# Kernel optimization log

Hardware: AMD Instinct MI355X
Metric: run time of the kernel (lower is better)

## Reference

```python
import jax, jax.numpy as jnp
import numpy as np

NUM_HEADS = 4
NUM_GROUPS = 8
EPS = 1e-5


def group_norm(x, gamma, beta):
    B, C, H, W = x.shape
    xg = x.reshape(B, NUM_GROUPS, C // NUM_GROUPS, H, W)
    mean = xg.mean(axis=(2, 3, 4), keepdims=True)
    var = xg.var(axis=(2, 3, 4), keepdims=True)
    xn = ((xg - mean) * jax.lax.rsqrt(var + EPS)).reshape(B, C, H, W)
    return xn * gamma[None, :, None, None] + beta[None, :, None, None]


def setup_inputs() -> dict:
    key = jax.random.key(0)
    k1, k2, k3 = jax.random.split(key, 3)
    B, C, H, W = 16, 512, 32, 32
    x = jax.random.normal(k1, (B, C, H, W), dtype=jnp.float32)
    gn_gamma = jnp.ones((C,), dtype=jnp.float32)
    gn_beta = jnp.zeros((C,), dtype=jnp.float32)
    w_qkv = jax.random.normal(k2, (3 * C, C), dtype=jnp.float32) * 0.02
    w_proj = jax.random.normal(k3, (C, C), dtype=jnp.float32) * 0.02
    b_proj = jnp.zeros((C,), dtype=jnp.float32)
    return {"x": x, "gn_gamma": gn_gamma, "gn_beta": gn_beta,
            "w_qkv": w_qkv, "w_proj": w_proj, "b_proj": b_proj}


def reference(x, gn_gamma, gn_beta, w_qkv, w_proj, b_proj):
    B, C, H, W = x.shape
    nh = NUM_HEADS
    hd = C // nh
    N = H * W

    x_norm = group_norm(x, gn_gamma, gn_beta)
    # 1x1 conv == channel matmul: (B,C,H,W) x (3C,C) -> (B,3C,H,W)
    qkv = jnp.einsum('bchw,dc->bdhw', x_norm, w_qkv)
    qkv = qkv.reshape(B, 3, nh, hd, N)
    q, k, v = qkv[:, 0], qkv[:, 1], qkv[:, 2]  # each (B, nh, hd, N)

    scale = hd ** (-0.5)
    attn = jnp.einsum('bhci,bhcj->bhij', q, k) * scale  # (B, nh, N, N)
    attn = jax.nn.softmax(attn, axis=-1)
    out = jnp.einsum('bhij,bhcj->bhci', attn, v)  # (B, nh, hd, N)
    out = out.reshape(B, C, H, W)

    proj = jnp.einsum('bchw,dc->bdhw', out, w_proj) + b_proj[None, :, None, None]
    return x + proj
```

## Files before the change

kernel.cpp:

```cpp
#include <hip/hip_runtime.h>
#include <stdint.h>

typedef unsigned short u16;
typedef unsigned int u32;
typedef __attribute__((ext_vector_type(8))) short short8;
typedef __attribute__((ext_vector_type(4))) float f32x4;
typedef __attribute__((ext_vector_type(16))) float f32x16;
typedef __attribute__((ext_vector_type(4))) u32 u32x4;

#define BATCH 16
#define CCH   512
#define NPIX  1024
#define NGRP  8
#define CPG   64
#define NHEAD 4
#define HDIM  128
#define KVBLK 64

__device__ __forceinline__ u16 f2bf(float f) {
  union { float f; u32 u; } v; v.f = f;
  u32 u = v.u;
  u32 r = (u + 0x7FFFu + ((u >> 16) & 1u)) >> 16;
  return (u16)r;
}

__device__ __forceinline__ void gload16(const void* g, void* l) {
  typedef __attribute__((address_space(3))) u32 L;
  typedef __attribute__((address_space(1))) const u32 G;
  __builtin_amdgcn_global_load_lds((G*)(uintptr_t)g, (L*)(u32)(uintptr_t)l, 16, 0, 0);
}

#define CVTPK(dst, a, b) asm("v_cvt_pk_bf16_f32 %0, %1, %2" : "=v"(dst) : "v"(a), "v"(b))
#define PLSWAP(a, b) asm("v_permlane32_swap_b32 %0, %1" : "+v"(a), "+v"(b))

__device__ __forceinline__ short8 rd512(const char* base, int r, int ck, int hi) {
  int byte = ((r >> 2) * 512) +
             ((((r & 3) * 128) + ck * 32 + hi * 16) ^ (((r >> 2) & 15) << 4));
  return *reinterpret_cast<const short8*>(base + byte);
}

__device__ __forceinline__ float softmax_pack(const f32x16& s0, const f32x16& s1, short8* pf) {
  float ps[4] = {0.f, 0.f, 0.f, 0.f};
  u32 pw[16];
  #pragma unroll
  for (int u = 0; u < 8; ++u) {
    float pa = exp2f(s0[2*u]);  float pb = exp2f(s0[2*u+1]);
    float pc = exp2f(s1[2*u]);  float pd = exp2f(s1[2*u+1]);
    ps[u & 3] += (pa + pb) + (pc + pd);
    CVTPK(pw[u],     pa, pb);
    CVTPK(pw[8 + u], pc, pd);
  }
  PLSWAP(pw[0], pw[2]);  PLSWAP(pw[1], pw[3]);
  PLSWAP(pw[4], pw[6]);  PLSWAP(pw[5], pw[7]);
  PLSWAP(pw[8], pw[10]); PLSWAP(pw[9], pw[11]);
  PLSWAP(pw[12], pw[14]); PLSWAP(pw[13], pw[15]);
  #pragma unroll
  for (int f = 0; f < 4; ++f) {
    u32x4 t = {pw[f*4], pw[f*4+1], pw[f*4+2], pw[f*4+3]};
    pf[f] = __builtin_bit_cast(short8, t);
  }
  float psum = (ps[0] + ps[1]) + (ps[2] + ps[3]);
  psum += __shfl_xor(psum, 32);
  return psum;
}

__global__ void gn_stats_k(const float* __restrict__ x, float* __restrict__ part) {
  int bg = blockIdx.x >> 3, sl = blockIdx.x & 7;
  const float* p = x + (size_t)bg * (CPG * NPIX) + sl * 8192;
  float s = 0.f, ss = 0.f;
  for (int i = threadIdx.x; i < 2048; i += 256) {
    float4 v = reinterpret_cast<const float4*>(p)[i];
    s  += v.x + v.y + v.z + v.w;
    ss += v.x*v.x + v.y*v.y + v.z*v.z + v.w*v.w;
  }
  for (int o = 32; o > 0; o >>= 1) { s += __shfl_down(s, o); ss += __shfl_down(ss, o); }
  __shared__ float sh[8];
  int wid = threadIdx.x >> 6;
  if ((threadIdx.x & 63) == 0) { sh[wid*2] = s; sh[wid*2+1] = ss; }
  __syncthreads();
  if (threadIdx.x == 0) {
    part[blockIdx.x*2]   = sh[0]+sh[2]+sh[4]+sh[6];
    part[blockIdx.x*2+1] = sh[1]+sh[3]+sh[5]+sh[7];
  }
}

__global__ __launch_bounds__(256) void gn_apply_t(const float* __restrict__ x,
                                                  const float* __restrict__ gamma,
                                                  const float* __restrict__ beta,
                                                  const float* __restrict__ part,
                                                  u16* __restrict__ xnT) {
  const int p0 = blockIdx.x * 64;
  const int c0 = blockIdx.y * 64;
  const int b  = blockIdx.z;
  __shared__ float lt[64][66];

  const int bg = b * NGRP + (c0 >> 6);
  float s = 0.f, ss = 0.f;
  #pragma unroll
  for (int k2 = 0; k2 < 8; ++k2) { s += part[(bg*8 + k2)*2]; ss += part[(bg*8 + k2)*2 + 1]; }
  const float invn = 1.f / (float)(CPG * NPIX);
  const float mean = s * invn;
  const float rstd = rsqrtf(ss * invn - mean * mean + 1e-5f);

  const int t = threadIdx.x;
  #pragma unroll
  for (int pass = 0; pass < 4; ++pass) {
    int c   = c0 + (t >> 4) + pass * 16;
    int pix = p0 + (t & 15) * 4;
    float ga = gamma[c] * rstd;
    float be = beta[c] - mean * ga;
    float4 v = *reinterpret_cast<const float4*>(&x[((size_t)(b*CCH + c)) * NPIX + pix]);
    int pl = (t & 15) * 4, cl = (t >> 4) + pass * 16;
    lt[pl+0][cl] = v.x*ga + be;
    lt[pl+1][cl] = v.y*ga + be;
    lt[pl+2][cl] = v.z*ga + be;
    lt[pl+3][cl] = v.w*ga + be;
  }
  __syncthreads();
  const int pl = t >> 2, cq = (t & 3) * 16;
  u32 wbuf[8];
  #pragma unroll
  for (int e = 0; e < 8; ++e) {
    u16 lo = f2bf(lt[pl][cq + e*2]);
    u16 hi = f2bf(lt[pl][cq + e*2 + 1]);
    wbuf[e] = (u32)lo | ((u32)hi << 16);
  }
  u32* dst = (u32*)&xnT[((size_t)(b*NPIX + p0 + pl)) * CCH + c0 + cq];
  #pragma unroll
  for (int e = 0; e < 8; ++e) dst[e] = wbuf[e];
}

__global__ void f2bf_all(const float* __restrict__ wqkv, const float* __restrict__ wproj,
                         u16* __restrict__ wq, u16* __restrict__ wp, float qs) {
  int i = blockIdx.x * 256 + threadIdx.x;
  float4 v; u16* dst; float sc = 1.f;
  if (i < 196608) {
    v = reinterpret_cast<const float4*>(wqkv)[i];
    if (i < 65536) sc = qs;
    dst = wq + (size_t)i * 4;
  } else {
    v = reinterpret_cast<const float4*>(wproj)[i - 196608];
    dst = wp + (size_t)(i - 196608) * 4;
  }
  u32 lo = (u32)f2bf(v.x*sc) | ((u32)f2bf(v.y*sc) << 16);
  u32 hi = (u32)f2bf(v.z*sc) | ((u32)f2bf(v.w*sc) << 16);
  *reinterpret_cast<uint2*>(dst) = make_uint2(lo, hi);
}

__global__ __launch_bounds__(256, 2) void gemm_qkv(const u16* __restrict__ xnT,
                                                   const u16* __restrict__ wq_bf,
                                                   u16* __restrict__ outQ,
                                                   u16* __restrict__ outK,
                                                   u16* __restrict__ outV) {
  __shared__ __align__(16) char smem[65536];

  const int id = blockIdx.x;
  const int wg = (id & 7) * 192 + (id >> 3);
  const bool mode0 = (wg < 1024);
  int rt, ct;
  if (mode0) { rt = wg >> 3; ct = wg & 7; }
  else       { int w1 = wg - 1024; rt = w1 & 3; ct = w1 >> 2; }

  const char* Ab = mode0 ? (const char*)xnT + (size_t)rt * 131072
                         : (const char*)wq_bf + (size_t)(8 + rt) * 131072;
  const char* Bb = mode0 ? (const char*)wq_bf + (size_t)ct * 131072
                         : (const char*)xnT + (size_t)ct * 131072;

  const int t = threadIdx.x;
  const int lane = t & 63, w = t >> 6;
  const int q = lane & 31, hi = lane >> 5;
  const int rh = (w >> 1) * 64, ch = (w & 1) * 64;

  int soff[4];
  #pragma unroll
  for (int i = 0; i < 4; ++i) {
    int p = w*4096 + i*1024 + lane*16;
    int lrow = p >> 9, off = p & 511;
    int loff = off ^ ((lrow & 15) << 4);
    soff[i] = (lrow*4 + (loff >> 7)) * 1024 + (loff & 127);
  }

  #pragma unroll
  for (int i = 0; i < 4; ++i) {
    gload16(Ab + soff[i], smem +         w*4096 + i*1024);
    gload16(Bb + soff[i], smem + 16384 + w*4096 + i*1024);
  }

  f32x16 acc[2][2] = {};

  for (int kt = 0; kt < 8; ++kt) {
    asm volatile("s_waitcnt vmcnt(0)" ::: "memory");
    __syncthreads();
    const char* cur = smem + (kt & 1) * 32768;
    if (kt + 1 < 8) {
      char* nxt = smem + ((kt + 1) & 1) * 32768;
      #pragma unroll
      for (int i = 0; i < 4; ++i) {
        gload16(Ab + (kt+1)*128 + soff[i], nxt +         w*4096 + i*1024);
        gload16(Bb + (kt+1)*128 + soff[i], nxt + 16384 + w*4096 + i*1024);
      }
    }
    __builtin_amdgcn_s_setprio(1);
    #pragma unroll
    for (int ck = 0; ck < 4; ++ck) {
      short8 af0 = rd512(cur,         rh + q,      ck, hi);
      short8 af1 = rd512(cur,         rh + 32 + q, ck, hi);
      short8 bf0 = rd512(cur + 16384, ch + q,      ck, hi);
      short8 bf1 = rd512(cur + 16384, ch + 32 + q, ck, hi);
      acc[0][0] = __builtin_amdgcn_mfma_f32_32x32x16_bf16(af0, bf0, acc[0][0], 0, 0, 0);
      acc[0][1] = __builtin_amdgcn_mfma_f32_32x32x16_bf16(af0, bf1, acc[0][1], 0, 0, 0);
      acc[1][0] = __builtin_amdgcn_mfma_f32_32x32x16_bf16(af1, bf0, acc[1][0], 0, 0, 0);
      acc[1][1] = __builtin_amdgcn_mfma_f32_32x32x16_bf16(af1, bf1, acc[1][1], 0, 0, 0);
    }
    __builtin_amdgcn_s_setprio(0);
  }

  __syncthreads();
  u16* Dt = (u16*)smem;
  #pragma unroll
  for (int r = 0; r < 16; ++r) {
    int ar = (r & 3) + 8*(r >> 2) + 4*hi;
    Dt[(rh +      ar) * 136 + ch +      q] = f2bf(acc[0][0][r]);
    Dt[(rh +      ar) * 136 + ch + 32 + q] = f2bf(acc[0][1][r]);
    Dt[(rh + 32 + ar) * 136 + ch +      q] = f2bf(acc[1][0][r]);
    Dt[(rh + 32 + ar) * 136 + ch + 32 + q] = f2bf(acc[1][1][r]);
  }
  __syncthreads();

  const int rl = t >> 1, hoff = (t & 1) * 64;
  uint4 buf[8];
  const uint4* s4 = reinterpret_cast<const uint4*>(&Dt[rl*136 + hoff]);
  #pragma unroll
  for (int e = 0; e < 8; ++e) buf[e] = s4[e];

  u16* gdst;
  if (mode0) {
    const int tok0 = rt * 128;
    const int b = tok0 >> 10, pix0 = tok0 & 1023;
    const int h = ct & 3;
    u16* base = (ct >= 4) ? outK : outQ;
    gdst = base + ((size_t)((b*NHEAD + h)) * NPIX + pix0 + rl) * HDIM + hoff;
  } else {
    const int m0 = rt * 128, tok0 = ct * 128;
    const int b = tok0 >> 10, pix0 = tok0 & 1023;
    gdst = outV + ((size_t)(b*CCH + m0 + rl)) * NPIX + pix0 + hoff;
  }
  uint4* g4 = reinterpret_cast<uint4*>(gdst);
  #pragma unroll
  for (int e = 0; e < 8; ++e) g4[e] = buf[e];
}

__global__ __launch_bounds__(256, 2) void gemm_proj(const u16* __restrict__ wp_bf,
                                                    const u16* __restrict__ attnO,
                                                    const float* __restrict__ xres,
                                                    const float* __restrict__ bias,
                                                    float* __restrict__ outF) {
  __shared__ __align__(16) char smem[65536];

  const int id = blockIdx.x;
  const int wg = (id & 7) * 64 + (id >> 3);
  const int rt = wg & 3, ct = wg >> 2;

  const char* Ab = (const char*)wp_bf + (size_t)rt * 131072;
  const char* Bb = (const char*)attnO + (size_t)ct * 131072;

  const int t = threadIdx.x;
  const int lane = t & 63, w = t >> 6;
  const int q = lane & 31, hi = lane >> 5;
  const int rh = (w >> 1) * 64, ch = (w & 1) * 64;

  int soff[4];
  #pragma unroll
  for (int i = 0; i < 4; ++i) {
    int p = w*4096 + i*1024 + lane*16;
    int lrow = p >> 9, off = p & 511;
    int loff = off ^ ((lrow & 15) << 4);
    soff[i] = (lrow*4 + (loff >> 7)) * 1024 + (loff & 127);
  }

  #pragma unroll
  for (int i = 0; i < 4; ++i) {
    gload16(Ab + soff[i], smem +         w*4096 + i*1024);
    gload16(Bb + soff[i], smem + 16384 + w*4096 + i*1024);
  }

  f32x16 acc[2][2] = {};

  for (int kt = 0; kt < 8; ++kt) {
    asm volatile("s_waitcnt vmcnt(0)" ::: "memory");
    __syncthreads();
    const char* cur = smem + (kt & 1) * 32768;
    if (kt + 1 < 8) {
      char* nxt = smem + ((kt + 1) & 1) * 32768;
      #pragma unroll
      for (int i = 0; i < 4; ++i) {
        gload16(Ab + (kt+1)*128 + soff[i], nxt +         w*4096 + i*1024);
        gload16(Bb + (kt+1)*128 + soff[i], nxt + 16384 + w*4096 + i*1024);
      }
    }
    __builtin_amdgcn_s_setprio(1);
    #pragma unroll
    for (int ck = 0; ck < 4; ++ck) {
      short8 af0 = rd512(cur,         rh + q,      ck, hi);
      short8 af1 = rd512(cur,         rh + 32 + q, ck, hi);
      short8 bf0 = rd512(cur + 16384, ch + q,      ck, hi);
      short8 bf1 = rd512(cur + 16384, ch + 32 + q, ck, hi);
      acc[0][0] = __builtin_amdgcn_mfma_f32_32x32x16_bf16(af0, bf0, acc[0][0], 0, 0, 0);
      acc[0][1] = __builtin_amdgcn_mfma_f32_32x32x16_bf16(af0, bf1, acc[0][1], 0, 0, 0);
      acc[1][0] = __builtin_amdgcn_mfma_f32_32x32x16_bf16(af1, bf0, acc[1][0], 0, 0, 0);
      acc[1][1] = __builtin_amdgcn_mfma_f32_32x32x16_bf16(af1, bf1, acc[1][1], 0, 0, 0);
    }
    __builtin_amdgcn_s_setprio(0);
  }

  const int m0 = rt * 128, tok0 = ct * 128;
  const int b = tok0 >> 10, pix0 = tok0 & 1023;
  #pragma unroll
  for (int r = 0; r < 16; ++r) {
    int ar = (r & 3) + 8*(r >> 2) + 4*hi;
    int m0r = m0 + rh + ar, m1r = m0 + rh + 32 + ar;
    size_t o00 = ((size_t)(b*CCH + m0r)) * NPIX + pix0 + ch + q;
    size_t o01 = o00 + 32;
    size_t o10 = ((size_t)(b*CCH + m1r)) * NPIX + pix0 + ch + q;
    size_t o11 = o10 + 32;
    outF[o00] = xres[o00] + acc[0][0][r] + bias[m0r];
    outF[o01] = xres[o01] + acc[0][1][r] + bias[m0r];
    outF[o10] = xres[o10] + acc[1][0][r] + bias[m1r];
    outF[o11] = xres[o11] + acc[1][1][r] + bias[m1r];
  }
}

__global__ __launch_bounds__(256, 2) void attn_k(const u16* __restrict__ Qt,
                                                 const u16* __restrict__ Kt,
                                                 const u16* __restrict__ Vb,
                                                 u16* __restrict__ attnO) {
  int id = blockIdx.x;
  int swz = (id & 7) * 64 + (id >> 3);
  const int qt = swz & 7;
  const int h  = (swz >> 3) & 3;
  const int b  = swz >> 5;
  const int bh = b * NHEAD + h;

  __shared__ __align__(16) char smem[65536];

  const int t = threadIdx.x;
  const int lane = t & 63, w = t >> 6;
  const int q = lane & 31, hi = lane >> 5;

  const u16*  Qb    = Qt + ((size_t)bh * NPIX + qt*128 + w*32 + q) * HDIM;
  const char* Kbase = (const char*)(Kt + (size_t)bh * NPIX * HDIM);
  const char* Vbase = (const char*)(Vb + ((size_t)b*CCH + h*HDIM) * NPIX);

  short8 qf[8];
  #pragma unroll
  for (int ck = 0; ck < 8; ++ck)
    qf[ck] = *reinterpret_cast<const short8*>(&Qb[ck*16 + hi*8]);

  int koff[4], voff[4];
  #pragma unroll
  for (int i = 0; i < 4; ++i) {
    int d = w*4096 + i*1024 + lane*16;
    int r = d >> 8, cb = d & 255;
    int col = cb ^ ((r & 15) << 4);
    koff[i] = r*256 + col;
    int half = col >> 7, kvb = col & 127;
    voff[i] = (2*r + half)*2048 + kvb;
  }

  const int ksw = (q & 15) << 4;
  const int vsw = (q >> 1) << 4;

  f32x16 of[4] = {};
  float l_run = 0.f;
  short8 pf[4];

  #pragma unroll
  for (int i = 0; i < 4; ++i) {
    gload16(Kbase + koff[i],                  smem +         w*4096 + i*1024);
    gload16(Vbase + voff[i],                  smem + 32768 + w*4096 + i*1024);
    gload16(Kbase + (size_t)64*256 + koff[i], smem + 16384 + w*4096 + i*1024);
  }
  asm volatile("s_waitcnt vmcnt(0)" ::: "memory");
  __syncthreads();

  {
    f32x16 sn[2] = {};
    #pragma unroll
    for (int ck = 0; ck < 8; ++ck) {
      const short8 kf0 = *reinterpret_cast<const short8*>(smem + q*256      + ((ck*32 + hi*16) ^ ksw));
      const short8 kf1 = *reinterpret_cast<const short8*>(smem + (32+q)*256 + ((ck*32 + hi*16) ^ ksw));
      sn[0] = __builtin_amdgcn_mfma_f32_32x32x16_bf16(kf0, qf[ck], sn[0], 0, 0, 0);
      sn[1] = __builtin_amdgcn_mfma_f32_32x32x16_bf16(kf1, qf[ck], sn[1], 0, 0, 0);
    }
    l_run += softmax_pack(sn[0], sn[1], pf);
  }

  for (int tt = 0; tt < 16; ++tt) {
    asm volatile("s_waitcnt vmcnt(0)" ::: "memory");
    __syncthreads();

    const char* kcur = smem + (((tt+1) & 1) << 14);
    const char* vcur = smem + 32768 + ((tt & 1) << 14);

    if (tt + 1 < 16) {
      char* vdst = smem + 32768 + (((tt+1) & 1) << 14);
      #pragma unroll
      for (int i = 0; i < 4; ++i)
        gload16(Vbase + (size_t)(tt+1)*128 + voff[i], vdst + w*4096 + i*1024);
    }
    if (tt + 2 < 16) {
      char* kdst = smem + ((tt & 1) << 14);
      #pragma unroll
      for (int i = 0; i < 4; ++i)
        gload16(Kbase + (size_t)(tt+2)*64*256 + koff[i], kdst + w*4096 + i*1024);
    }

    f32x16 sn[2] = {};
    __builtin_amdgcn_s_setprio(1);
    if (tt + 1 < 16) {
      #pragma unroll
      for (int ck = 0; ck < 8; ++ck) {
        const short8 kf0 = *reinterpret_cast<const short8*>(kcur + q*256      + ((ck*32 + hi*16) ^ ksw));
        const short8 kf1 = *reinterpret_cast<const short8*>(kcur + (32+q)*256 + ((ck*32 + hi*16) ^ ksw));
        sn[0] = __builtin_amdgcn_mfma_f32_32x32x16_bf16(kf0, qf[ck], sn[0], 0, 0, 0);
        sn[1] = __builtin_amdgcn_mfma_f32_32x32x16_bf16(kf1, qf[ck], sn[1], 0, 0, 0);
      }
    }
    #pragma unroll
    for (int cg = 0; cg < 4; ++cg) {
      const char* vrow = vcur + (cg*16 + (q >> 1))*256;
      const int hb = (q & 1) << 7;
      #pragma unroll
      for (int kc = 0; kc < 4; ++kc)
        of[cg] = __builtin_amdgcn_mfma_f32_32x32x16_bf16(
            *reinterpret_cast<const short8*>(vrow + ((hb + kc*32 + hi*16) ^ vsw)),
            pf[kc], of[cg], 0, 0, 0);
    }
    __builtin_amdgcn_s_setprio(0);

    if (tt + 1 < 16)
      l_run += softmax_pack(sn[0], sn[1], pf);
  }

  float inv = 1.f / l_run;
  u16* orow = attnO + ((size_t)(b*NPIX + qt*128 + w*32 + q)) * CCH + h*HDIM;
  #pragma unroll
  for (int cg = 0; cg < 4; ++cg) {
    #pragma unroll
    for (int u = 0; u < 8; ++u) {
      int c = cg*32 + ((2*u) & 3) + 8*(u >> 1) + 4*hi;
      u32 pk = (u32)f2bf(of[cg][2*u] * inv) | ((u32)f2bf(of[cg][2*u+1] * inv) << 16);
      *reinterpret_cast<u32*>(&orow[c]) = pk;
    }
  }
}

extern "C" void kernel_launch(void* const* d_in, const int* in_sizes, int n_in,
                              void* d_out, int out_size, void* d_ws, size_t ws_size,
                              hipStream_t stream) {
  const float* x     = (const float*)d_in[0];
  const float* gamma = (const float*)d_in[1];
  const float* beta  = (const float*)d_in[2];
  const float* wqkv  = (const float*)d_in[3];
  const float* wproj = (const float*)d_in[4];
  const float* bproj = (const float*)d_in[5];
  float* out = (float*)d_out;

  char* ws = (char*)d_ws;
  float* part   = (float*)ws;
  u16*   xnT    = (u16*)(ws + 8192);
  u16*   wq_bf  = (u16*)(ws + 8192 + (16u<<20));
  u16*   wp_bf  = (u16*)((char*)wq_bf + 1572864);
  u16*   Qt     = (u16*)((char*)wp_bf + 524288);
  u16*   Kt     = (u16*)((char*)Qt + (16u<<20));
  u16*   Vb     = (u16*)((char*)Kt + (16u<<20));
  u16*   attnO  = (u16*)((char*)Vb + (16u<<20));

  const float qs = 0.08838834764831845f * 1.44269504088896f;

  gn_stats_k<<<dim3(1024), dim3(256), 0, stream>>>(x, part);
  gn_apply_t<<<dim3(16, 8, BATCH), dim3(256), 0, stream>>>(x, gamma, beta, part, xnT);
  f2bf_all<<<dim3(1024), dim3(256), 0, stream>>>(wqkv, wproj, wq_bf, wp_bf, qs);

  gemm_qkv<<<dim3(1536), dim3(256), 0, stream>>>(xnT, wq_bf, Qt, Kt, Vb);

  attn_k<<<dim3(512), dim3(256), 0, stream>>>(Qt, Kt, Vb, attnO);

  gemm_proj<<<dim3(512), dim3(256), 0, stream>>>(wp_bf, attnO, x, bproj, out);
}
```

Baseline: 123.3 us.

## Split attention KV range in two blocks and add a combine kernel

The attention kernel now splits the 1024 keys into two halves processed by separate blocks, doubling the grid to 1024 blocks, halving the per-block LDS footprint, and allowing 4 blocks per CU. Each half writes unnormalized bf16 partial outputs and row sums, and a new combine kernel adds them, normalizes and writes the attention output in the layout the projection GEMM expects. This targets better occupancy and latency hiding, at the cost of an extra launch, extra global traffic for partials, and rounding partials to bf16 before summation. There is no running-max subtraction, so it relies on pre-scaled logits staying bounded, as the original code also did.

```diff
diff --git a/kernel.cpp b/kernel.cpp
--- a/kernel.cpp
+++ b/kernel.cpp
@@ -15,7 +15,6 @@
 #define CPG   64
 #define NHEAD 4
 #define HDIM  128
-#define KVBLK 64
 
 __device__ __forceinline__ u16 f2bf(float f) {
   union { float f; u32 u; } v; v.f = f;
@@ -23,6 +22,12 @@
   u32 r = (u + 0x7FFFu + ((u >> 16) & 1u)) >> 16;
   return (u16)r;
 }
+__device__ __forceinline__ float bf2f_lo(u32 w) {
+  union { u32 u; float f; } v; v.u = w << 16; return v.f;
+}
+__device__ __forceinline__ float bf2f_hi(u32 w) {
+  union { u32 u; float f; } v; v.u = w & 0xFFFF0000u; return v.f;
+}
 
 __device__ __forceinline__ void gload16(const void* g, void* l) {
   typedef __attribute__((address_space(3))) u32 L;
@@ -39,29 +44,23 @@
   return *reinterpret_cast<const short8*>(base + byte);
 }
 
-__device__ __forceinline__ float softmax_pack(const f32x16& s0, const f32x16& s1, short8* pf) {
-  float ps[4] = {0.f, 0.f, 0.f, 0.f};
-  u32 pw[16];
+__device__ __forceinline__ float softmax_pack32(const f32x16& sn, short8* pf) {
+  float ps = 0.f;
+  u32 pw[8];
   #pragma unroll
   for (int u = 0; u < 8; ++u) {
-    float pa = exp2f(s0[2*u]);  float pb = exp2f(s0[2*u+1]);
-    float pc = exp2f(s1[2*u]);  float pd = exp2f(s1[2*u+1]);
-    ps[u & 3] += (pa + pb) + (pc + pd);
-    CVTPK(pw[u],     pa, pb);
-    CVTPK(pw[8 + u], pc, pd);
-  }
-  PLSWAP(pw[0], pw[2]);  PLSWAP(pw[1], pw[3]);
-  PLSWAP(pw[4], pw[6]);  PLSWAP(pw[5], pw[7]);
-  PLSWAP(pw[8], pw[10]); PLSWAP(pw[9], pw[11]);
-  PLSWAP(pw[12], pw[14]); PLSWAP(pw[13], pw[15]);
-  #pragma unroll
-  for (int f = 0; f < 4; ++f) {
-    u32x4 t = {pw[f*4], pw[f*4+1], pw[f*4+2], pw[f*4+3]};
-    pf[f] = __builtin_bit_cast(short8, t);
-  }
-  float psum = (ps[0] + ps[1]) + (ps[2] + ps[3]);
-  psum += __shfl_xor(psum, 32);
-  return psum;
+    float pa = exp2f(sn[2*u]);
+    float pb = exp2f(sn[2*u+1]);
+    ps += pa + pb;
+    CVTPK(pw[u], pa, pb);
+  }
+  PLSWAP(pw[0], pw[2]); PLSWAP(pw[1], pw[3]);
+  PLSWAP(pw[4], pw[6]); PLSWAP(pw[5], pw[7]);
+  u32x4 t0 = {pw[0], pw[1], pw[2], pw[3]};
+  u32x4 t1 = {pw[4], pw[5], pw[6], pw[7]};
+  pf[0] = __builtin_bit_cast(short8, t0);
+  pf[1] = __builtin_bit_cast(short8, t1);
+  return ps;
 }
 
 __global__ void gn_stats_k(const float* __restrict__ x, float* __restrict__ part) {
@@ -330,129 +329,151 @@
   }
 }
 
-__global__ __launch_bounds__(256, 2) void attn_k(const u16* __restrict__ Qt,
+__global__ __launch_bounds__(256, 4) void attn_k(const u16* __restrict__ Qt,
                                                  const u16* __restrict__ Kt,
                                                  const u16* __restrict__ Vb,
-                                                 u16* __restrict__ attnO) {
+                                                 u16* __restrict__ Opart,
+                                                 float* __restrict__ lpart) {
   int id = blockIdx.x;
-  int swz = (id & 7) * 64 + (id >> 3);
-  const int qt = swz & 7;
-  const int h  = (swz >> 3) & 3;
-  const int b  = swz >> 5;
-  const int bh = b * NHEAD + h;
-
-  __shared__ __align__(16) char smem[65536];
+  int swz = (id & 7) * 128 + (id >> 3);
+  const int half = swz & 1;
+  const int qt   = (swz >> 1) & 7;
+  const int h    = (swz >> 4) & 3;
+  const int b    = swz >> 6;
+  const int bh   = b * NHEAD + h;
+
+  __shared__ __align__(16) char smem[32768];
 
   const int t = threadIdx.x;
   const int lane = t & 63, w = t >> 6;
   const int q = lane & 31, hi = lane >> 5;
 
   const u16*  Qb    = Qt + ((size_t)bh * NPIX + qt*128 + w*32 + q) * HDIM;
-  const char* Kbase = (const char*)(Kt + (size_t)bh * NPIX * HDIM);
-  const char* Vbase = (const char*)(Vb + ((size_t)b*CCH + h*HDIM) * NPIX);
+  const char* Kbase = (const char*)(Kt + (size_t)bh * NPIX * HDIM) + half * (512*256);
+  const char* Vbase = (const char*)(Vb + ((size_t)b*CCH + h*HDIM) * NPIX) + half * 1024;
 
   short8 qf[8];
   #pragma unroll
   for (int ck = 0; ck < 8; ++ck)
     qf[ck] = *reinterpret_cast<const short8*>(&Qb[ck*16 + hi*8]);
 
-  int koff[4], voff[4];
-  #pragma unroll
-  for (int i = 0; i < 4; ++i) {
-    int d = w*4096 + i*1024 + lane*16;
+  int koff[2], voff[2];
+  #pragma unroll
+  for (int i = 0; i < 2; ++i) {
+    int d = (i*256 + t) * 16;
     int r = d >> 8, cb = d & 255;
     int col = cb ^ ((r & 15) << 4);
     koff[i] = r*256 + col;
-    int half = col >> 7, kvb = col & 127;
-    voff[i] = (2*r + half)*2048 + kvb;
-  }
+    int c = (col >> 6)*32 + r;
+    voff[i] = c*2048 + (col & 63);
+  }
+  const int ldst0 = w*1024;
 
   const int ksw = (q & 15) << 4;
-  const int vsw = (q >> 1) << 4;
 
   f32x16 of[4] = {};
-  float l_run = 0.f;
-  short8 pf[4];
-
-  #pragma unroll
-  for (int i = 0; i < 4; ++i) {
-    gload16(Kbase + koff[i],                  smem +         w*4096 + i*1024);
-    gload16(Vbase + voff[i],                  smem + 32768 + w*4096 + i*1024);
-    gload16(Kbase + (size_t)64*256 + koff[i], smem + 16384 + w*4096 + i*1024);
+  float lsum = 0.f;
+  short8 pf[2];
+
+  #pragma unroll
+  for (int i = 0; i < 2; ++i) {
+    gload16(Kbase + koff[i],            smem +          i*4096 + ldst0);
+    gload16(Vbase + voff[i],            smem + 16384 +  i*4096 + ldst0);
+    gload16(Kbase + 32*256 + koff[i],   smem +  8192 +  i*4096 + ldst0);
   }
   asm volatile("s_waitcnt vmcnt(0)" ::: "memory");
   __syncthreads();
 
   {
-    f32x16 sn[2] = {};
+    f32x16 sn = {};
     #pragma unroll
     for (int ck = 0; ck < 8; ++ck) {
-      const short8 kf0 = *reinterpret_cast<const short8*>(smem + q*256      + ((ck*32 + hi*16) ^ ksw));
-      const short8 kf1 = *reinterpret_cast<const short8*>(smem + (32+q)*256 + ((ck*32 + hi*16) ^ ksw));
-      sn[0] = __builtin_amdgcn_mfma_f32_32x32x16_bf16(kf0, qf[ck], sn[0], 0, 0, 0);
-      sn[1] = __builtin_amdgcn_mfma_f32_32x32x16_bf16(kf1, qf[ck], sn[1], 0, 0, 0);
-    }
-    l_run += softmax_pack(sn[0], sn[1], pf);
+      const short8 kf = *reinterpret_cast<const short8*>(smem + q*256 + ((ck*32 + hi*16) ^ ksw));
+      sn = __builtin_amdgcn_mfma_f32_32x32x16_bf16(kf, qf[ck], sn, 0, 0, 0);
+    }
+    lsum += softmax_pack32(sn, pf);
   }
 
   for (int tt = 0; tt < 16; ++tt) {
     asm volatile("s_waitcnt vmcnt(0)" ::: "memory");
     __syncthreads();
 
-    const char* kcur = smem + (((tt+1) & 1) << 14);
-    const char* vcur = smem + 32768 + ((tt & 1) << 14);
+    const char* kcur = smem + (((tt+1) & 1) << 13);
+    const char* vcur = smem + 16384 + ((tt & 1) << 13);
 
     if (tt + 1 < 16) {
-      char* vdst = smem + 32768 + (((tt+1) & 1) << 14);
+      char* vdst = smem + 16384 + (((tt+1) & 1) << 13);
       #pragma unroll
-      for (int i = 0; i < 4; ++i)
-        gload16(Vbase + (size_t)(tt+1)*128 + voff[i], vdst + w*4096 + i*1024);
+      for (int i = 0; i < 2; ++i)
+        gload16(Vbase + (size_t)(tt+1)*64 + voff[i], vdst + i*4096 + ldst0);
     }
     if (tt + 2 < 16) {
-      char* kdst = smem + ((tt & 1) << 14);
+      char* kdst = smem + ((tt & 1) << 13);
       #pragma unroll
-      for (int i = 0; i < 4; ++i)
-        gload16(Kbase + (size_t)(tt+2)*64*256 + koff[i], kdst + w*4096 + i*1024);
-    }
-
-    f32x16 sn[2] = {};
+      for (int i = 0; i < 2; ++i)
+        gload16(Kbase + (size_t)(tt+2)*32*256 + koff[i], kdst + i*4096 + ldst0);
+    }
+
+    f32x16 sn = {};
     __builtin_amdgcn_s_setprio(1);
     if (tt + 1 < 16) {
       #pragma unroll
       for (int ck = 0; ck < 8; ++ck) {
-        const short8 kf0 = *reinterpret_cast<const short8*>(kcur + q*256      + ((ck*32 + hi*16) ^ ksw));
-        const short8 kf1 = *reinterpret_cast<const short8*>(kcur + (32+q)*256 + ((ck*32 + hi*16) ^ ksw));
-        sn[0] = __builtin_amdgcn_mfma_f32_32x32x16_bf16(kf0, qf[ck], sn[0], 0, 0, 0);
-        sn[1] = __builtin_amdgcn_mfma_f32_32x32x16_bf16(kf1, qf[ck], sn[1], 0, 0, 0);
+        const short8 kf = *reinterpret_cast<const short8*>(kcur + q*256 + ((ck*32 + hi*16) ^ ksw));
+        sn = __builtin_amdgcn_mfma_f32_32x32x16_bf16(kf, qf[ck], sn, 0, 0, 0);
       }
     }
     #pragma unroll
     for (int cg = 0; cg < 4; ++cg) {
-      const char* vrow = vcur + (cg*16 + (q >> 1))*256;
-      const int hb = (q & 1) << 7;
       #pragma unroll
-      for (int kc = 0; kc < 4; ++kc)
+      for (int kc = 0; kc < 2; ++kc)
         of[cg] = __builtin_amdgcn_mfma_f32_32x32x16_bf16(
-            *reinterpret_cast<const short8*>(vrow + ((hb + kc*32 + hi*16) ^ vsw)),
+            *reinterpret_cast<const short8*>(vcur + q*256 + ((cg*64 + kc*32 + hi*16) ^ ksw)),
             pf[kc], of[cg], 0, 0, 0);
     }
     __builtin_amdgcn_s_setprio(0);
 
     if (tt + 1 < 16)
-      l_run += softmax_pack(sn[0], sn[1], pf);
-  }
-
-  float inv = 1.f / l_run;
-  u16* orow = attnO + ((size_t)(b*NPIX + qt*128 + w*32 + q)) * CCH + h*HDIM;
+      lsum += softmax_pack32(sn, pf);
+  }
+
+  const int qrow = qt*128 + w*32 + q;
+  u16* orow = Opart + ((size_t)(half*64 + bh) * NPIX + qrow) * HDIM;
   #pragma unroll
   for (int cg = 0; cg < 4; ++cg) {
     #pragma unroll
     for (int u = 0; u < 8; ++u) {
       int c = cg*32 + ((2*u) & 3) + 8*(u >> 1) + 4*hi;
-      u32 pk = (u32)f2bf(of[cg][2*u] * inv) | ((u32)f2bf(of[cg][2*u+1] * inv) << 16);
+      u32 pk = (u32)f2bf(of[cg][2*u]) | ((u32)f2bf(of[cg][2*u+1]) << 16);
       *reinterpret_cast<u32*>(&orow[c]) = pk;
     }
   }
+  lsum += __shfl_xor(lsum, 32);
+  if (lane < 32)
+    lpart[(size_t)(half*64 + bh) * NPIX + qrow] = lsum;
+}
+
+__global__ void attn_combine(const u16* __restrict__ Opart, const float* __restrict__ lpart,
+                             u16* __restrict__ attnO) {
+  int g = blockIdx.x * 256 + threadIdx.x;
+  int qi = g >> 4;
+  int seg = (g & 15) * 8;
+  const uint4 a = *reinterpret_cast<const uint4*>(Opart + ((size_t)qi) * HDIM + seg);
+  const uint4 c = *reinterpret_cast<const uint4*>(Opart + ((size_t)(qi + 65536)) * HDIM + seg);
+  float inv = 1.f / (lpart[qi] + lpart[qi + 65536]);
+  u32 aw[4] = {a.x, a.y, a.z, a.w};
+  u32 cw[4] = {c.x, c.y, c.z, c.w};
+  u32 ow[4];
+  #pragma unroll
+  for (int e = 0; e < 4; ++e) {
+    float lo = (bf2f_lo(aw[e]) + bf2f_lo(cw[e])) * inv;
+    float hi = (bf2f_hi(aw[e]) + bf2f_hi(cw[e])) * inv;
+    ow[e] = (u32)f2bf(lo) | ((u32)f2bf(hi) << 16);
+  }
+  int bh = qi >> 10, qq = qi & 1023;
+  int bb = bh >> 2, hh = bh & 3;
+  u16* dst = attnO + ((size_t)(bb * NPIX + qq)) * CCH + hh * HDIM + seg;
+  *reinterpret_cast<uint4*>(dst) = make_uint4(ow[0], ow[1], ow[2], ow[3]);
 }
 
 extern "C" void kernel_launch(void* const* d_in, const int* in_sizes, int n_in,
@@ -475,8 +496,14 @@
   u16*   Kt     = (u16*)((char*)Qt + (16u<<20));
   u16*   Vb     = (u16*)((char*)Kt + (16u<<20));
   u16*   attnO  = (u16*)((char*)Vb + (16u<<20));
+  u16*   Opart1 = (u16*)((char*)attnO + (16u<<20));
+  float* lpart  = (float*)((char*)Opart1 + (16u<<20));
+  u16*   Opart  = xnT;
 
   const float qs = 0.08838834764831845f * 1.44269504088896f;
+  (void)Opart1;
+  u16* OpartBase = attnO;
+  u16* attnO2    = (u16*)((char*)lpart + 524288);
 
   gn_stats_k<<<dim3(1024), dim3(256), 0, stream>>>(x, part);
   gn_apply_t<<<dim3(16, 8, BATCH), dim3(256), 0, stream>>>(x, gamma, beta, part, xnT);
@@ -484,7 +511,9 @@
 
   gemm_qkv<<<dim3(1536), dim3(256), 0, stream>>>(xnT, wq_bf, Qt, Kt, Vb);
 
-  attn_k<<<dim3(512), dim3(256), 0, stream>>>(Qt, Kt, Vb, attnO);
-
-  gemm_proj<<<dim3(512), dim3(256), 0, stream>>>(wp_bf, attnO, x, bproj, out);
-}
+  attn_k<<<dim3(1024), dim3(256), 0, stream>>>(Qt, Kt, Vb, OpartBase, lpart);
+
+  attn_combine<<<dim3(4096), dim3(256), 0, stream>>>(OpartBase, lpart, attnO2);
+
+  gemm_proj<<<dim3(512), dim3(256), 0, stream>>>(wp_bf, attnO2, x, bproj, out);
+}
```

Measured after the change: 147.3 us. 19.4% more time.
